# Optimization experiments

Measured on AMD Instinct MI355X. Metric: run time of the kernel, lower is better.

Reference implementation:

```python
import jax, jax.numpy as jnp
import numpy as np

B, K, L = 2048, 8, 256
H1, H2 = 18, 12  # hidden sizes of each tiny per-feature MLP (1->18->12->1)
EPS = 1e-8


def setup_inputs() -> dict:
    key = jax.random.key(0)
    k0, k1, k2, k3, k4, k5, k6 = jax.random.split(key, 7)
    s1 = 1.0 / np.sqrt(1.0)
    s2 = 1.0 / np.sqrt(H1)
    s3 = 1.0 / np.sqrt(H2)
    return {
        "x": jax.random.normal(k0, (B, K, L), dtype=jnp.float32),
        "W1": jax.random.normal(k1, (K, L, H1), dtype=jnp.float32) * s1,
        "b1": jax.random.normal(k2, (K, L, H1), dtype=jnp.float32) * s1,
        "W2": jax.random.normal(k3, (K, L, H1, H2), dtype=jnp.float32) * s2,
        "b2": jax.random.normal(k4, (K, L, H2), dtype=jnp.float32) * s2,
        "W3": jax.random.normal(k5, (K, L, H2), dtype=jnp.float32) * s3,
        "b3": jax.random.normal(k6, (K, L), dtype=jnp.float32) * s3,
    }


def reference(x, W1, b1, W2, b2, W3, b3):
    # standardize each (k, l) feature over the batch dimension
    mu = jnp.mean(x, axis=0, keepdims=True)              # [1,K,L]
    sd = jnp.std(x, axis=0, keepdims=True)               # [1,K,L]
    xs = (x - mu) / (sd + EPS)                           # [B,K,L]
    # all K*L tiny MLPs as batched contractions (grouped-GEMM view)
    h1 = jax.nn.relu(xs[..., None] * W1 + b1)            # [B,K,L,H1]
    h2 = jax.nn.relu(jnp.einsum("bklh,klhj->bklj", h1, W2) + b2)  # [B,K,L,H2]
    out = jnp.einsum("bklj,klj->bkl", h2, W3) + b3       # [B,K,L]
    return out
```

## Files before the change

kernel.cpp:

```cpp
#include <hip/hip_runtime.h>
#include <hip/hip_fp16.h>

typedef _Float16 half8  __attribute__((ext_vector_type(8)));
typedef _Float16 half4  __attribute__((ext_vector_type(4)));
typedef _Float16 h2v    __attribute__((ext_vector_type(2)));
typedef __fp16   fp16x2 __attribute__((ext_vector_type(2)));
typedef float    f32x4  __attribute__((ext_vector_type(4)));

#define B_N    2048
#define KLTOT  2048
#define NCHUNK 128
#define CHUNK_ROWS 16
#define XCS    580
#define LJS2   36

__device__ __forceinline__ int hmap(int g, int e) {
    return (g < 2) ? ((e < 5) ? g * 5 + e : -1)
                   : ((e < 4) ? 10 + (g - 2) * 4 + e : -1);
}

__device__ __forceinline__ unsigned int f16b(float f) {
    union { _Float16 h; unsigned short u; } c;
    c.h = (_Float16)f;
    return (unsigned int)c.u;
}

__global__ __launch_bounds__(256) void stats_partial(const float* __restrict__ x,
                                                     float* __restrict__ part) {
    int c4 = blockIdx.x * 256 + threadIdx.x;
    int chunk = blockIdx.y;
    const float4* p = (const float4*)(x + (size_t)(chunk * CHUNK_ROWS) * KLTOT) + c4;
    float4 s = {0.f, 0.f, 0.f, 0.f}, s2 = {0.f, 0.f, 0.f, 0.f};
#pragma unroll
    for (int r = 0; r < CHUNK_ROWS; ++r) {
        float4 v = p[(size_t)r * (KLTOT / 4)];
        s.x += v.x; s.y += v.y; s.z += v.z; s.w += v.w;
        s2.x = fmaf(v.x, v.x, s2.x); s2.y = fmaf(v.y, v.y, s2.y);
        s2.z = fmaf(v.z, v.z, s2.z); s2.w = fmaf(v.w, v.w, s2.w);
    }
    float4* o = (float4*)(part + ((size_t)chunk * KLTOT + (size_t)c4 * 4) * 2);
    float4 o0 = {s.x, s2.x, s.y, s2.y};
    float4 o1 = {s.z, s2.z, s.w, s2.w};
    o[0] = o0;
    o[1] = o1;
}

__global__ __launch_bounds__(512, 4) void fused_main(
    const float* __restrict__ x,
    const float* __restrict__ part,
    const float* __restrict__ W1, const float* __restrict__ b1,
    const float* __restrict__ W2, const float* __restrict__ b2,
    const float* __restrict__ W3, const float* __restrict__ b3,
    float* __restrict__ out)
{
    __shared__ float        xt[16 * XCS];
    __shared__ unsigned int afb[16 * 256];
    __shared__ float        red[512][2];
    __shared__ unsigned int w1h[16][16], b1h[16][16], w3h[16][8];
    __shared__ float        b2f[16][16], smu[16], srs[16], sb3v[16];

    const int tid = threadIdx.x;
    const int bid = blockIdx.x;
    const int nf  = (bid & 7) * 64 + (bid >> 3);
    const int cgp = nf & 127, rg = nf >> 7;
    const int cols0 = cgp * 16, rows0 = rg * 512;

    {
        const int c = tid & 15, q = tid >> 4;
        float s = 0.f, s2 = 0.f;
#pragma unroll
        for (int m = 0; m < 4; ++m) {
            float2 v = *(const float2*)&part[((size_t)(q + 32 * m) * KLTOT + cols0 + c) * 2];
            s += v.x; s2 += v.y;
        }
        red[tid][0] = s; red[tid][1] = s2;
    }
    {
        const int c = tid & 15, rr = tid >> 4;
#pragma unroll
        for (int i = 0; i < 16; ++i) {
            int r = rr * 16 + i;
            xt[c * XCS + i * LJS2 + rr] = x[(size_t)(rows0 + r) * KLTOT + cols0 + c];
        }
    }
    __syncthreads();

    if (tid < 16) {
        float S = 0.f, S2 = 0.f;
#pragma unroll 8
        for (int m = 0; m < 32; ++m) {
            S  += red[tid + 16 * m][0];
            S2 += red[tid + 16 * m][1];
        }
        float mu  = S / (float)B_N;
        float var = fmaxf(S2 / (float)B_N - mu * mu, 0.f);
        smu[tid]  = mu;
        srs[tid]  = 1.f / (sqrtf(var) + 1e-8f);
        sb3v[tid] = b3[cols0 + tid];
    }
    {
        float* W2tmp = (float*)afb;
        const float4* src = (const float4*)(W2 + (size_t)cols0 * 216);
        for (int i = tid; i < 864; i += 512)
            ((float4*)W2tmp)[i] = src[i];
    }
    __syncthreads();

    unsigned int dw[8];
    {
        const float* W2tmp = (const float*)afb;
        const int col = tid >> 5, d0 = (tid & 31) * 8;
#pragma unroll
        for (int k = 0; k < 8; ++k) {
            int d = d0 + k;
            unsigned int u[2];
#pragma unroll
            for (int h = 0; h < 2; ++h) {
                int idx = d * 2 + h;
                int gg = idx >> 7, j = (idx >> 3) & 15, e = idx & 7;
                int hh = hmap(gg, e);
                float v = (hh >= 0 && j < 12) ? W2tmp[col * 216 + hh * 12 + j] : 0.f;
                u[h] = f16b(v);
            }
            dw[k] = u[0] | (u[1] << 16);
        }
    }
    if (tid < 256) {
        int c2 = tid >> 4, l = tid & 15;
        int gg = l >> 2, q = l & 3;
        unsigned int wu = 0, bu = 0;
        if (q < 3) {
            float mu = smu[c2], rs = srs[c2];
            float w0 = 0.f, b0 = 0.f, w1v = 0.f, b1v = 0.f;
            int h0 = hmap(gg, q * 2), h1_ = hmap(gg, q * 2 + 1);
            if (h0 >= 0) {
                w0 = W1[(size_t)(cols0 + c2) * 18 + h0] * rs;
                b0 = fmaf(-mu, w0, b1[(size_t)(cols0 + c2) * 18 + h0]);
            }
            if (h1_ >= 0) {
                w1v = W1[(size_t)(cols0 + c2) * 18 + h1_] * rs;
                b1v = fmaf(-mu, w1v, b1[(size_t)(cols0 + c2) * 18 + h1_]);
            }
            wu = f16b(w0) | (f16b(w1v) << 16);
            bu = f16b(b0) | (f16b(b1v) << 16);
        }
        w1h[c2][l] = wu;
        b1h[c2][l] = bu;
        b2f[c2][l] = (l < 12) ? b2[(size_t)(cols0 + c2) * 12 + l] : 0.f;
    } else if (tid < 384) {
        int t2 = tid - 256;
        int c2 = t2 >> 3, l = t2 & 7;
        int j0 = 2 * l, j1 = 2 * l + 1;
        float v0 = (j0 < 12) ? W3[(size_t)(cols0 + c2) * 12 + j0] : 0.f;
        float v1 = (j1 < 12) ? W3[(size_t)(cols0 + c2) * 12 + j1] : 0.f;
        w3h[c2][l] = f16b(v0) | (f16b(v1) << 16);
    }
    __syncthreads();

    {
        const int col = tid >> 5, d0 = (tid & 31) * 8;
#pragma unroll
        for (int k = 0; k < 8; ++k)
            afb[col * 256 + d0 + k] = dw[k];
    }
    __syncthreads();

    const int w = tid >> 6, l = tid & 63;
    const int g = l >> 4, lj = l & 15;
    const h2v z2 = {(_Float16)0.f, (_Float16)0.f};
    const f32x4 zc = {0.f, 0.f, 0.f, 0.f};

#pragma unroll
    for (int half = 0; half < 2; ++half) {
        const int cl = w + half * 8;

        union { uint4 u; half8 h; } af;
        af.u = *(const uint4*)&afb[cl * 256 + (g * 16 + lj) * 4];
        union { uint4 u; h2v p[4]; } w1u, b1u;
        w1u.u = *(const uint4*)&w1h[cl][g * 4];
        b1u.u = *(const uint4*)&b1h[cl][g * 4];
        union { uint2 u; half4 h; } a2;
        a2.u = *(const uint2*)&w3h[cl][g * 2];
        f32x4 b2r = *(const f32x4*)&b2f[cl][g * 4];
        float b3v = sb3v[cl];

        float res[8];
        const float* xb = &xt[cl * XCS + lj * LJS2];
#pragma unroll
        for (int rbq = 0; rbq < 4; ++rbq) {
            f32x4 xa = *(const f32x4*)(xb + rbq * 8);
            f32x4 xc = *(const f32x4*)(xb + rbq * 8 + 4);
#pragma unroll
            for (int k = 0; k < 8; ++k) {
                float xsv = (k < 4) ? xa[k & 3] : xc[k & 3];
                _Float16 xh = (_Float16)xsv;
                h2v x2 = {xh, xh};
                union { h2v p[4]; half8 h; } bf;
                bf.p[0] = __builtin_elementwise_max(x2 * w1u.p[0] + b1u.p[0], z2);
                bf.p[1] = __builtin_elementwise_max(x2 * w1u.p[1] + b1u.p[1], z2);
                bf.p[2] = __builtin_elementwise_max(x2 * w1u.p[2] + b1u.p[2], z2);
                bf.p[3] = z2;

                f32x4 acc = __builtin_amdgcn_mfma_f32_16x16x32_f16(af.h, bf.h, b2r, 0, 0, 0);

                union { fp16x2 c[2]; half4 h; } zf;
                zf.c[0] = __builtin_amdgcn_cvt_pkrtz(fmaxf(acc[0], 0.f), fmaxf(acc[1], 0.f));
                zf.c[1] = __builtin_amdgcn_cvt_pkrtz(fmaxf(acc[2], 0.f), fmaxf(acc[3], 0.f));

                f32x4 acc2 = __builtin_amdgcn_mfma_f32_16x16x16f16(a2.h, zf.h, zc, 0, 0, 0);

                if (rbq == g) res[k] = acc2[0] + b3v;
            }
        }
        float* tb = &xt[cl * XCS + lj * LJS2 + g * 8];
        f32x4 r0 = { res[0], res[1], res[2], res[3] };
        f32x4 r1 = { res[4], res[5], res[6], res[7] };
        *(f32x4*)tb = r0;
        *(f32x4*)(tb + 4) = r1;
    }
    __syncthreads();

#pragma unroll
    for (int p = 0; p < 4; ++p) {
        int idx = p * 512 + tid;
        int c4 = idx & 3, r = idx >> 2;
        int base = (r & 15) * LJS2 + (r >> 4);
        f32x4 v;
#pragma unroll
        for (int e = 0; e < 4; ++e)
            v[e] = xt[(c4 * 4 + e) * XCS + base];
        *(f32x4*)(out + (size_t)(rows0 + r) * KLTOT + cols0 + c4 * 4) = v;
    }
}

extern "C" void kernel_launch(void* const* d_in, const int* in_sizes, int n_in,
                              void* d_out, int out_size, void* d_ws, size_t ws_size,
                              hipStream_t stream) {
    const float* x  = (const float*)d_in[0];
    const float* W1 = (const float*)d_in[1];
    const float* b1 = (const float*)d_in[2];
    const float* W2 = (const float*)d_in[3];
    const float* b2 = (const float*)d_in[4];
    const float* W3 = (const float*)d_in[5];
    const float* b3 = (const float*)d_in[6];
    float* out  = (float*)d_out;
    float* part = (float*)d_ws;

    stats_partial<<<dim3(2, NCHUNK), 256, 0, stream>>>(x, part);
    fused_main   <<<dim3(512),       512, 0, stream>>>(x, part, W1, b1, W2, b2, W3, b3, out);
}
```

Measured before the change: 30.92 us.

## Fuse batch-stats pass into main kernel via grid-wide atomic barrier

Removes the separate stats_partial kernel. Each block now computes partial sums while staging its x tile, publishes them to workspace, and signals an atomic counter. It overlaps weight staging and the W2 repacking with the wait, then spins until all 512 blocks arrive before finalizing mean and std. This saves a kernel launch and a second read of x, but it adds a memset, relies on all 512 blocks being co-resident, and drops the XCD-aware block remapping.

```diff
diff --git a/kernel.cpp b/kernel.cpp
--- a/kernel.cpp
+++ b/kernel.cpp
@@ -9,8 +9,7 @@
 
 #define B_N    2048
 #define KLTOT  2048
-#define NCHUNK 128
-#define CHUNK_ROWS 16
+#define NBLK   512
 #define XCS    580
 #define LJS2   36
 
@@ -25,32 +24,12 @@
     return (unsigned int)c.u;
 }
 
-__global__ __launch_bounds__(256) void stats_partial(const float* __restrict__ x,
-                                                     float* __restrict__ part) {
-    int c4 = blockIdx.x * 256 + threadIdx.x;
-    int chunk = blockIdx.y;
-    const float4* p = (const float4*)(x + (size_t)(chunk * CHUNK_ROWS) * KLTOT) + c4;
-    float4 s = {0.f, 0.f, 0.f, 0.f}, s2 = {0.f, 0.f, 0.f, 0.f};
-#pragma unroll
-    for (int r = 0; r < CHUNK_ROWS; ++r) {
-        float4 v = p[(size_t)r * (KLTOT / 4)];
-        s.x += v.x; s.y += v.y; s.z += v.z; s.w += v.w;
-        s2.x = fmaf(v.x, v.x, s2.x); s2.y = fmaf(v.y, v.y, s2.y);
-        s2.z = fmaf(v.z, v.z, s2.z); s2.w = fmaf(v.w, v.w, s2.w);
-    }
-    float4* o = (float4*)(part + ((size_t)chunk * KLTOT + (size_t)c4 * 4) * 2);
-    float4 o0 = {s.x, s2.x, s.y, s2.y};
-    float4 o1 = {s.z, s2.z, s.w, s2.w};
-    o[0] = o0;
-    o[1] = o1;
-}
-
-__global__ __launch_bounds__(512, 4) void fused_main(
+__global__ __launch_bounds__(512, 4) void fused_all(
     const float* __restrict__ x,
-    const float* __restrict__ part,
     const float* __restrict__ W1, const float* __restrict__ b1,
     const float* __restrict__ W2, const float* __restrict__ b2,
     const float* __restrict__ W3, const float* __restrict__ b3,
+    float* __restrict__ part, unsigned int* __restrict__ cnt,
     float* __restrict__ out)
 {
     __shared__ float        xt[16 * XCS];
@@ -61,27 +40,20 @@
 
     const int tid = threadIdx.x;
     const int bid = blockIdx.x;
-    const int nf  = (bid & 7) * 64 + (bid >> 3);
-    const int cgp = nf & 127, rg = nf >> 7;
+    const int cgp = bid & 127, rg = bid >> 7;
     const int cols0 = cgp * 16, rows0 = rg * 512;
 
     {
-        const int c = tid & 15, q = tid >> 4;
+        const int c = tid & 15, rr = tid >> 4;
         float s = 0.f, s2 = 0.f;
-#pragma unroll
-        for (int m = 0; m < 4; ++m) {
-            float2 v = *(const float2*)&part[((size_t)(q + 32 * m) * KLTOT + cols0 + c) * 2];
-            s += v.x; s2 += v.y;
-        }
-        red[tid][0] = s; red[tid][1] = s2;
-    }
-    {
-        const int c = tid & 15, rr = tid >> 4;
 #pragma unroll
         for (int i = 0; i < 16; ++i) {
             int r = rr * 16 + i;
-            xt[c * XCS + i * LJS2 + rr] = x[(size_t)(rows0 + r) * KLTOT + cols0 + c];
-        }
+            float v = x[(size_t)(rows0 + r) * KLTOT + cols0 + c];
+            s += v; s2 = fmaf(v, v, s2);
+            xt[c * XCS + i * LJS2 + rr] = v;
+        }
+        red[tid][0] = s; red[tid][1] = s2;
     }
     __syncthreads();
 
@@ -92,60 +64,35 @@
             S  += red[tid + 16 * m][0];
             S2 += red[tid + 16 * m][1];
         }
-        float mu  = S / (float)B_N;
-        float var = fmaxf(S2 / (float)B_N - mu * mu, 0.f);
-        smu[tid]  = mu;
-        srs[tid]  = 1.f / (sqrtf(var) + 1e-8f);
-        sb3v[tid] = b3[cols0 + tid];
-    }
+        float2 o = { S, S2 };
+        *(float2*)&part[((size_t)rg * KLTOT + cols0 + tid) * 2] = o;
+        __threadfence();
+    }
+    __syncthreads();
+    if (tid == 0)
+        __hip_atomic_fetch_add(cnt, 1u, __ATOMIC_RELEASE, __HIP_MEMORY_SCOPE_AGENT);
+
     {
         float* W2tmp = (float*)afb;
         const float4* src = (const float4*)(W2 + (size_t)cols0 * 216);
         for (int i = tid; i < 864; i += 512)
             ((float4*)W2tmp)[i] = src[i];
     }
-    __syncthreads();
-
-    unsigned int dw[8];
-    {
-        const float* W2tmp = (const float*)afb;
-        const int col = tid >> 5, d0 = (tid & 31) * 8;
-#pragma unroll
-        for (int k = 0; k < 8; ++k) {
-            int d = d0 + k;
-            unsigned int u[2];
-#pragma unroll
-            for (int h = 0; h < 2; ++h) {
-                int idx = d * 2 + h;
-                int gg = idx >> 7, j = (idx >> 3) & 15, e = idx & 7;
-                int hh = hmap(gg, e);
-                float v = (hh >= 0 && j < 12) ? W2tmp[col * 216 + hh * 12 + j] : 0.f;
-                u[h] = f16b(v);
-            }
-            dw[k] = u[0] | (u[1] << 16);
-        }
-    }
+    float w1r0 = 0.f, w1r1 = 0.f, b1r0 = 0.f, b1r1 = 0.f;
     if (tid < 256) {
         int c2 = tid >> 4, l = tid & 15;
         int gg = l >> 2, q = l & 3;
-        unsigned int wu = 0, bu = 0;
         if (q < 3) {
-            float mu = smu[c2], rs = srs[c2];
-            float w0 = 0.f, b0 = 0.f, w1v = 0.f, b1v = 0.f;
             int h0 = hmap(gg, q * 2), h1_ = hmap(gg, q * 2 + 1);
             if (h0 >= 0) {
-                w0 = W1[(size_t)(cols0 + c2) * 18 + h0] * rs;
-                b0 = fmaf(-mu, w0, b1[(size_t)(cols0 + c2) * 18 + h0]);
+                w1r0 = W1[(size_t)(cols0 + c2) * 18 + h0];
+                b1r0 = b1[(size_t)(cols0 + c2) * 18 + h0];
             }
             if (h1_ >= 0) {
-                w1v = W1[(size_t)(cols0 + c2) * 18 + h1_] * rs;
-                b1v = fmaf(-mu, w1v, b1[(size_t)(cols0 + c2) * 18 + h1_]);
-            }
-            wu = f16b(w0) | (f16b(w1v) << 16);
-            bu = f16b(b0) | (f16b(b1v) << 16);
-        }
-        w1h[c2][l] = wu;
-        b1h[c2][l] = bu;
+                w1r1 = W1[(size_t)(cols0 + c2) * 18 + h1_];
+                b1r1 = b1[(size_t)(cols0 + c2) * 18 + h1_];
+            }
+        }
         b2f[c2][l] = (l < 12) ? b2[(size_t)(cols0 + c2) * 12 + l] : 0.f;
     } else if (tid < 384) {
         int t2 = tid - 256;
@@ -154,14 +101,73 @@
         float v0 = (j0 < 12) ? W3[(size_t)(cols0 + c2) * 12 + j0] : 0.f;
         float v1 = (j1 < 12) ? W3[(size_t)(cols0 + c2) * 12 + j1] : 0.f;
         w3h[c2][l] = f16b(v0) | (f16b(v1) << 16);
-    }
-    __syncthreads();
-
+    } else if (tid < 400) {
+        sb3v[tid - 384] = b3[cols0 + tid - 384];
+    }
+    __syncthreads();
+
+    unsigned int dw[8];
+    {
+        const float* W2tmp = (const float*)afb;
+        const int col = tid >> 5, d0 = (tid & 31) * 8;
+#pragma unroll
+        for (int k = 0; k < 8; ++k) {
+            int d = d0 + k;
+            unsigned int u[2];
+#pragma unroll
+            for (int h = 0; h < 2; ++h) {
+                int idx = d * 2 + h;
+                int gg = idx >> 7, j = (idx >> 3) & 15, e = idx & 7;
+                int hh = hmap(gg, e);
+                float v = (hh >= 0 && j < 12) ? W2tmp[col * 216 + hh * 12 + j] : 0.f;
+                u[h] = f16b(v);
+            }
+            dw[k] = u[0] | (u[1] << 16);
+        }
+    }
+    __syncthreads();
     {
         const int col = tid >> 5, d0 = (tid & 31) * 8;
 #pragma unroll
         for (int k = 0; k < 8; ++k)
             afb[col * 256 + d0 + k] = dw[k];
+    }
+
+    if (tid == 0) {
+        long it = 0;
+        while (__hip_atomic_load(cnt, __ATOMIC_ACQUIRE, __HIP_MEMORY_SCOPE_AGENT) < NBLK
+               && ++it < (1L << 30)) { }
+    }
+    __syncthreads();
+
+    if (tid < 16) {
+        (void)__hip_atomic_load(cnt, __ATOMIC_ACQUIRE, __HIP_MEMORY_SCOPE_AGENT);
+        float S = 0.f, S2 = 0.f;
+#pragma unroll
+        for (int q = 0; q < 4; ++q) {
+            float2 v = *(const float2*)&part[((size_t)q * KLTOT + cols0 + tid) * 2];
+            S += v.x; S2 += v.y;
+        }
+        float mu  = S / (float)B_N;
+        float var = fmaxf(S2 / (float)B_N - mu * mu, 0.f);
+        smu[tid] = mu;
+        srs[tid] = 1.f / (sqrtf(var) + 1e-8f);
+    }
+    __syncthreads();
+
+    if (tid < 256) {
+        int c2 = tid >> 4, l = tid & 15;
+        int q = l & 3;
+        unsigned int wu = 0, bu = 0;
+        if (q < 3) {
+            float mu = smu[c2], rs = srs[c2];
+            float w0 = w1r0 * rs, w1v = w1r1 * rs;
+            float b0 = fmaf(-mu, w0, b1r0), b1v = fmaf(-mu, w1v, b1r1);
+            wu = f16b(w0) | (f16b(w1v) << 16);
+            bu = f16b(b0) | (f16b(b1v) << 16);
+        }
+        w1h[c2][l] = wu;
+        b1h[c2][l] = bu;
     }
     __syncthreads();
 
@@ -243,9 +249,12 @@
     const float* b2 = (const float*)d_in[4];
     const float* W3 = (const float*)d_in[5];
     const float* b3 = (const float*)d_in[6];
-    float* out  = (float*)d_out;
-    float* part = (float*)d_ws;
-
-    stats_partial<<<dim3(2, NCHUNK), 256, 0, stream>>>(x, part);
-    fused_main   <<<dim3(512),       512, 0, stream>>>(x, part, W1, b1, W2, b2, W3, b3, out);
-}
+    float* out = (float*)d_out;
+
+    float*        part = (float*)d_ws;
+    unsigned int* cnt  = (unsigned int*)((char*)d_ws + 4 * 2048 * 2 * sizeof(float));
+
+    hipMemsetAsync(cnt, 0, sizeof(unsigned int), stream);
+    fused_all<<<dim3(NBLK), 512, 0, stream>>>(x, W1, b1, W2, b2, W3, b3,
+                                              part, cnt, out);
+}
```

Result: slower. 71.88 us (+132.5%).

## Halve rows per block, double grid, and simplify shared-memory tile layout

Applied to the files above, without the earlier changes.

Each block now processes 256 batch rows instead of 512, so the grid grows to 1024 blocks and launch bounds ask for 8 waves per SIMD. The x tile in shared memory switches from a blocked, padded layout to a simple column-major layout with stride 258. Each thread's MFMA loop shrinks to 16 row-chunks, and the half loop is no longer unrolled, which adds extra barriers around the result write-back. The aim is more parallelism and occupancy from smaller LDS and register use. In exchange, the per-block setup (stats reduction, weight staging) is repeated twice as often and there are more syncs.

```diff
diff --git a/kernel.cpp b/kernel.cpp
--- a/kernel.cpp
+++ b/kernel.cpp
@@ -11,8 +11,7 @@
 #define KLTOT  2048
 #define NCHUNK 128
 #define CHUNK_ROWS 16
-#define XCS    580
-#define LJS2   36
+#define CS2    258
 
 __device__ __forceinline__ int hmap(int g, int e) {
     return (g < 2) ? ((e < 5) ? g * 5 + e : -1)
@@ -45,7 +44,7 @@
     o[1] = o1;
 }
 
-__global__ __launch_bounds__(512, 4) void fused_main(
+__global__ __launch_bounds__(512, 8) void fused_main(
     const float* __restrict__ x,
     const float* __restrict__ part,
     const float* __restrict__ W1, const float* __restrict__ b1,
@@ -53,7 +52,7 @@
     const float* __restrict__ W3, const float* __restrict__ b3,
     float* __restrict__ out)
 {
-    __shared__ float        xt[16 * XCS];
+    __shared__ float        xt[16 * CS2];
     __shared__ unsigned int afb[16 * 256];
     __shared__ float        red[512][2];
     __shared__ unsigned int w1h[16][16], b1h[16][16], w3h[16][8];
@@ -61,9 +60,9 @@
 
     const int tid = threadIdx.x;
     const int bid = blockIdx.x;
-    const int nf  = (bid & 7) * 64 + (bid >> 3);
+    const int nf  = (bid & 7) * 128 + (bid >> 3);
     const int cgp = nf & 127, rg = nf >> 7;
-    const int cols0 = cgp * 16, rows0 = rg * 512;
+    const int cols0 = cgp * 16, rows0 = rg * 256;
 
     {
         const int c = tid & 15, q = tid >> 4;
@@ -78,9 +77,9 @@
     {
         const int c = tid & 15, rr = tid >> 4;
 #pragma unroll
-        for (int i = 0; i < 16; ++i) {
-            int r = rr * 16 + i;
-            xt[c * XCS + i * LJS2 + rr] = x[(size_t)(rows0 + r) * KLTOT + cols0 + c];
+        for (int i = 0; i < 8; ++i) {
+            int r = rr * 8 + i;
+            xt[c * CS2 + r] = x[(size_t)(rows0 + r) * KLTOT + cols0 + c];
         }
     }
     __syncthreads();
@@ -170,7 +169,7 @@
     const h2v z2 = {(_Float16)0.f, (_Float16)0.f};
     const f32x4 zc = {0.f, 0.f, 0.f, 0.f};
 
-#pragma unroll
+#pragma unroll 1
     for (int half = 0; half < 2; ++half) {
         const int cl = w + half * 8;
 
@@ -184,51 +183,45 @@
         f32x4 b2r = *(const f32x4*)&b2f[cl][g * 4];
         float b3v = sb3v[cl];
 
-        float res[8];
-        const float* xb = &xt[cl * XCS + lj * LJS2];
-#pragma unroll
-        for (int rbq = 0; rbq < 4; ++rbq) {
-            f32x4 xa = *(const f32x4*)(xb + rbq * 8);
-            f32x4 xc = *(const f32x4*)(xb + rbq * 8 + 4);
-#pragma unroll
-            for (int k = 0; k < 8; ++k) {
-                float xsv = (k < 4) ? xa[k & 3] : xc[k & 3];
-                _Float16 xh = (_Float16)xsv;
-                h2v x2 = {xh, xh};
-                union { h2v p[4]; half8 h; } bf;
-                bf.p[0] = __builtin_elementwise_max(x2 * w1u.p[0] + b1u.p[0], z2);
-                bf.p[1] = __builtin_elementwise_max(x2 * w1u.p[1] + b1u.p[1], z2);
-                bf.p[2] = __builtin_elementwise_max(x2 * w1u.p[2] + b1u.p[2], z2);
-                bf.p[3] = z2;
-
-                f32x4 acc = __builtin_amdgcn_mfma_f32_16x16x32_f16(af.h, bf.h, b2r, 0, 0, 0);
-
-                union { fp16x2 c[2]; half4 h; } zf;
-                zf.c[0] = __builtin_amdgcn_cvt_pkrtz(fmaxf(acc[0], 0.f), fmaxf(acc[1], 0.f));
-                zf.c[1] = __builtin_amdgcn_cvt_pkrtz(fmaxf(acc[2], 0.f), fmaxf(acc[3], 0.f));
-
-                f32x4 acc2 = __builtin_amdgcn_mfma_f32_16x16x16f16(a2.h, zf.h, zc, 0, 0, 0);
-
-                if (rbq == g) res[k] = acc2[0] + b3v;
-            }
-        }
-        float* tb = &xt[cl * XCS + lj * LJS2 + g * 8];
-        f32x4 r0 = { res[0], res[1], res[2], res[3] };
-        f32x4 r1 = { res[4], res[5], res[6], res[7] };
-        *(f32x4*)tb = r0;
-        *(f32x4*)(tb + 4) = r1;
-    }
-    __syncthreads();
-
-#pragma unroll
-    for (int p = 0; p < 4; ++p) {
+        float res[4];
+        const float* xb = &xt[cl * CS2 + lj];
+#pragma unroll
+        for (int rc = 0; rc < 16; ++rc) {
+            float xsv = xb[rc * 16];
+            _Float16 xh = (_Float16)xsv;
+            h2v x2 = {xh, xh};
+            union { h2v p[4]; half8 h; } bf;
+            bf.p[0] = __builtin_elementwise_max(x2 * w1u.p[0] + b1u.p[0], z2);
+            bf.p[1] = __builtin_elementwise_max(x2 * w1u.p[1] + b1u.p[1], z2);
+            bf.p[2] = __builtin_elementwise_max(x2 * w1u.p[2] + b1u.p[2], z2);
+            bf.p[3] = z2;
+
+            f32x4 acc = __builtin_amdgcn_mfma_f32_16x16x32_f16(af.h, bf.h, b2r, 0, 0, 0);
+
+            union { fp16x2 c[2]; half4 h; } zf;
+            zf.c[0] = __builtin_amdgcn_cvt_pkrtz(fmaxf(acc[0], 0.f), fmaxf(acc[1], 0.f));
+            zf.c[1] = __builtin_amdgcn_cvt_pkrtz(fmaxf(acc[2], 0.f), fmaxf(acc[3], 0.f));
+
+            f32x4 acc2 = __builtin_amdgcn_mfma_f32_16x16x16f16(a2.h, zf.h, zc, 0, 0, 0);
+
+            if ((rc >> 2) == g) res[rc & 3] = acc2[0] + b3v;
+        }
+        __syncthreads();
+        float* tb = &xt[cl * CS2 + lj];
+#pragma unroll
+        for (int m = 0; m < 4; ++m)
+            tb[(g * 4 + m) * 16] = res[m];
+        __syncthreads();
+    }
+
+#pragma unroll
+    for (int p = 0; p < 2; ++p) {
         int idx = p * 512 + tid;
         int c4 = idx & 3, r = idx >> 2;
-        int base = (r & 15) * LJS2 + (r >> 4);
         f32x4 v;
 #pragma unroll
         for (int e = 0; e < 4; ++e)
-            v[e] = xt[(c4 * 4 + e) * XCS + base];
+            v[e] = xt[(c4 * 4 + e) * CS2 + r];
         *(f32x4*)(out + (size_t)(rows0 + r) * KLTOT + cols0 + c4 * 4) = v;
     }
 }
@@ -247,5 +240,5 @@
     float* part = (float*)d_ws;
 
     stats_partial<<<dim3(2, NCHUNK), 256, 0, stream>>>(x, part);
-    fused_main   <<<dim3(512),       512, 0, stream>>>(x, part, W1, b1, W2, b2, W3, b3, out);
-}
+    fused_main   <<<dim3(1024),      512, 0, stream>>>(x, part, W1, b1, W2, b2, W3, b3, out);
+}
```

Result: slower. 34.85 us (+12.7%).
